# Kernel optimization log

Hardware: AMD Instinct MI355X
Metric: run time of the kernel (lower is better)

Reference implementation:

```python
import math
import jax, jax.numpy as jnp
import numpy as np

B, T, DM, H = 2, 2048, 512, 8
D = DM // H
PROB_SPARSE_FACTOR = 0.4


def setup_inputs() -> dict:
    key = jax.random.key(0)
    ks = jax.random.split(key, 11)
    s = DM ** -0.5
    return {
        "query": jax.random.normal(ks[0], (B, T, DM), jnp.float32),
        "key": jax.random.normal(ks[1], (B, T, DM), jnp.float32),
        "value": jax.random.normal(ks[2], (B, T, DM), jnp.float32),
        "Wq": jax.random.normal(ks[3], (DM, DM), jnp.float32) * s,
        "bq": jnp.zeros((DM,), jnp.float32),
        "Wk": jax.random.normal(ks[4], (DM, DM), jnp.float32) * s,
        "bk": jnp.zeros((DM,), jnp.float32),
        "Wv": jax.random.normal(ks[5], (DM, DM), jnp.float32) * s,
        "bv": jnp.zeros((DM,), jnp.float32),
        "Wo": jax.random.normal(ks[6], (DM, DM), jnp.float32) * s,
        "bo": jnp.zeros((DM,), jnp.float32),
    }


def reference(query, key, value, Wq, bq, Wk, bk, Wv, bv, Wo, bo):
    Bq, Tq, dm = query.shape
    Tk = key.shape[1]
    # projections (torch Linear: x @ W.T + b), split heads -> [B,H,T,D]
    q = (query @ Wq.T + bq).reshape(Bq, Tq, H, D).transpose(0, 2, 1, 3)
    k = (key @ Wk.T + bk).reshape(Bq, Tk, H, D).transpose(0, 2, 1, 3)
    v = (value @ Wv.T + bv).reshape(Bq, Tk, H, D).transpose(0, 2, 1, 3)
    scale = math.sqrt(D)

    # full scores for KL-based query selection
    scores_all = jnp.einsum("bhqd,bhkd->bhqk", q, k) / scale  # [B,H,Tq,Tk]
    probs = jax.nn.softmax(scores_all, axis=-1)
    log_uniform = math.log(1.0 / Tk + 1e-10)
    kl = jnp.sum(probs * (jnp.log(probs + 1e-10) - log_uniform), axis=-1)  # [B,H,Tq]

    u = int(min(PROB_SPARSE_FACTOR * math.log(Tk), Tq))  # static
    _, topk = jax.lax.top_k(kl, u)  # [B,H,u]

    # gather selected queries, reduced attention
    q_red = jnp.take_along_axis(q, topk[..., None], axis=2)  # [B,H,u,D]
    s = jnp.einsum("bhud,bhkd->bhuk", q_red, k) / scale
    s = jnp.clip(jnp.nan_to_num(s, nan=-10000.0), -10000.0, 10000.0)
    w = jax.nn.softmax(s, axis=-1)
    out_red = jnp.einsum("bhuk,bhkd->bhud", w, v)  # [B,H,u,D]

    # scatter back into zeros at selected query positions
    b_idx = jnp.arange(Bq)[:, None, None]
    h_idx = jnp.arange(H)[None, :, None]
    out = jnp.zeros((Bq, H, Tq, D), q.dtype).at[b_idx, h_idx, topk].set(out_red)

    out = out.transpose(0, 2, 1, 3).reshape(Bq, Tq, dm)
    return out @ Wo.T + bo
```

## Files before the change

kernel.cpp:

```cpp
#include <hip/hip_runtime.h>
#include <hip/hip_bf16.h>

#define TT 2048
#define DMM 512
#define HH 8
#define DH 64
#define NBH 16
#define UU 3

typedef unsigned short u16;
typedef short bf16x8 __attribute__((ext_vector_type(8)));
typedef float f32x4 __attribute__((ext_vector_type(4)));

#define W_ZS     0
#define W_SS     131072
#define W_OUTRED 262144
#define W_TOPK   265216
#define W_U16    265280
#define NPROJ 2097152
#define NW    786432
#define W_NEED_BYTES (265280*4 + 5*NPROJ*2 + 2*NW*2)

__global__ void canary_kernel(float* __restrict__ out, float code, int n)
{
    int i = blockIdx.x * 256 + threadIdx.x;
    if (i < n) out[i] = (i == 0) ? code : 0.f;
}

__device__ __forceinline__ float rc_bf(u16 hi, u16 lo)
{
    return __uint_as_float(((unsigned)hi) << 16) + __uint_as_float(((unsigned)lo) << 16);
}

__global__ __launch_bounds__(256) void wsplit_kernel(
    const float* __restrict__ Wq, const float* __restrict__ Wk,
    const float* __restrict__ Wv,
    u16* __restrict__ whi, u16* __restrict__ wlo)
{
    const int n1 = DMM * DMM;
    for (int i = blockIdx.x * 256 + threadIdx.x; i < 3 * n1; i += gridDim.x * 256) {
        const int z = i / n1, rem = i - z * n1;
        const float w = (z == 0 ? Wq : (z == 1 ? Wk : Wv))[rem];
        const unsigned u = __float_as_uint(w);
        const u16 hi = (u16)(u >> 16);
        const float hf = __uint_as_float(u & 0xFFFF0000u);
        whi[i] = hi;
        wlo[i] = (u16)(__float_as_uint(w - hf) >> 16);
    }
}

__global__ __launch_bounds__(256) void projM_kernel(
    const float* __restrict__ q, const float* __restrict__ k, const float* __restrict__ v,
    const u16* __restrict__ whi, const u16* __restrict__ wlo,
    const float* __restrict__ bq, const float* __restrict__ bk, const float* __restrict__ bv,
    u16* __restrict__ qhi, u16* __restrict__ qlo,
    u16* __restrict__ khi, u16* __restrict__ klo,
    u16* __restrict__ Vh)
{
    __shared__ u16 Ah[128][40], Al[128][40], Bh[64][40], Bl[64][40];

    const int z = blockIdx.z;
    const float *X, *Bi;
    if (z == 0)      { X = q; Bi = bq; }
    else if (z == 1) { X = k; Bi = bk; }
    else             { X = v; Bi = bv; }

    const int tid = threadIdx.x;
    const int m0 = blockIdx.x * 128;
    const int h  = blockIdx.y;
    const int n0 = h * 64;
    const int w  = tid >> 6;
    const int lane = tid & 63;
    const int fr = lane & 15;
    const int kg = lane >> 4;
    const int kb = kg * 8;

    const int sr = tid >> 1;
    const int sk = (tid & 1) * 16;
    const int wr = tid >> 2;
    const int wk = (tid & 3) * 8;

    f32x4 acc[2][4];
#pragma unroll
    for (int t = 0; t < 2; ++t)
#pragma unroll
        for (int j = 0; j < 4; ++j) acc[t][j] = (f32x4){0.f, 0.f, 0.f, 0.f};

    for (int k0 = 0; k0 < DMM; k0 += 32) {
        __syncthreads();
        {
            const float* p = X + (size_t)(m0 + sr) * DMM + k0 + sk;
            float xv[16];
#pragma unroll
            for (int i4 = 0; i4 < 4; ++i4) {
                float4 a = *(const float4*)(p + i4 * 4);
                xv[i4*4+0]=a.x; xv[i4*4+1]=a.y; xv[i4*4+2]=a.z; xv[i4*4+3]=a.w;
            }
            unsigned hb[16], lb[16];
#pragma unroll
            for (int i = 0; i < 16; ++i) {
                unsigned u = __float_as_uint(xv[i]);
                hb[i] = u >> 16;
                float hf = __uint_as_float(u & 0xFFFF0000u);
                lb[i] = __float_as_uint(xv[i] - hf) >> 16;
            }
#pragma unroll
            for (int half = 0; half < 2; ++half) {
                uint4 H, L;
                H.x = hb[half*8+0]|(hb[half*8+1]<<16); H.y = hb[half*8+2]|(hb[half*8+3]<<16);
                H.z = hb[half*8+4]|(hb[half*8+5]<<16); H.w = hb[half*8+6]|(hb[half*8+7]<<16);
                L.x = lb[half*8+0]|(lb[half*8+1]<<16); L.y = lb[half*8+2]|(lb[half*8+3]<<16);
                L.z = lb[half*8+4]|(lb[half*8+5]<<16); L.w = lb[half*8+6]|(lb[half*8+7]<<16);
                *(uint4*)&Ah[sr][sk + half*8] = H;
                *(uint4*)&Al[sr][sk + half*8] = L;
            }

            const size_t wi = ((size_t)z * DMM + n0 + wr) * DMM + k0 + wk;
            *(uint4*)&Bh[wr][wk] = *(const uint4*)(whi + wi);
            *(uint4*)&Bl[wr][wk] = *(const uint4*)(wlo + wi);
        }
        __syncthreads();

        bf16x8 ah[2], al[2];
#pragma unroll
        for (int t = 0; t < 2; ++t) {
            ah[t] = *(const bf16x8*)&Ah[w*32 + t*16 + fr][kb];
            al[t] = *(const bf16x8*)&Al[w*32 + t*16 + fr][kb];
        }
#pragma unroll
        for (int j = 0; j < 4; ++j) {
            bf16x8 bhf = *(const bf16x8*)&Bh[j*16 + fr][kb];
            bf16x8 blf = *(const bf16x8*)&Bl[j*16 + fr][kb];
#pragma unroll
            for (int t = 0; t < 2; ++t) {
                acc[t][j] = __builtin_amdgcn_mfma_f32_16x16x32_bf16(ah[t], bhf, acc[t][j], 0, 0, 0);
                acc[t][j] = __builtin_amdgcn_mfma_f32_16x16x32_bf16(ah[t], blf, acc[t][j], 0, 0, 0);
                acc[t][j] = __builtin_amdgcn_mfma_f32_16x16x32_bf16(al[t], bhf, acc[t][j], 0, 0, 0);
            }
        }
    }

#pragma unroll
    for (int t = 0; t < 2; ++t) {
#pragma unroll
        for (int j = 0; j < 4; ++j) {
            const int d = j*16 + fr;
            const float bias = Bi[n0 + d];
#pragma unroll
            for (int r = 0; r < 4; ++r) {
                const int row = m0 + w*32 + t*16 + kg*4 + r;
                const int bb  = row >> 11;
                const int tt  = row & 2047;
                const float val = acc[t][j][r] + bias;
                const size_t idx = ((size_t)(bb*HH + h) * TT + tt) * DH + d;
                const unsigned u = __float_as_uint(val);
                if (z == 2) {
                    Vh[idx] = (u16)((u + 0x7FFFu + ((u >> 16) & 1u)) >> 16);
                } else {
                    const u16 hi = (u16)(u >> 16);
                    const float hf = __uint_as_float(u & 0xFFFF0000u);
                    const u16 lo = (u16)(__float_as_uint(val - hf) >> 16);
                    if (z == 0) { qhi[idx] = hi; qlo[idx] = lo; }
                    else        { khi[idx] = hi; klo[idx] = lo; }
                }
            }
        }
    }
}

__global__ __launch_bounds__(256) void scoreM_kernel(
    const u16* __restrict__ qhi, const u16* __restrict__ qlo,
    const u16* __restrict__ khi, const u16* __restrict__ klo,
    float* __restrict__ zs, float* __restrict__ ss)
{
    __shared__ u16 Kh[64][76], Kl[64][76];

    const int qt = blockIdx.x, bh = blockIdx.y, zh = blockIdx.z;
    const int qr0 = qt * 128;
    const int tid = threadIdx.x;
    const int w  = tid >> 6;
    const int lane = tid & 63;
    const int fr = lane & 15;
    const int kg = lane >> 4;
    const int kb = kg * 8;

    bf16x8 qh0[2], qh1[2], ql0[2], ql1[2];
#pragma unroll
    for (int t = 0; t < 2; ++t) {
        const size_t qbase = ((size_t)bh*TT + qr0 + w*32 + t*16 + fr) * DH;
        qh0[t] = *(const bf16x8*)(qhi + qbase + kb);
        qh1[t] = *(const bf16x8*)(qhi + qbase + 32 + kb);
        ql0[t] = *(const bf16x8*)(qlo + qbase + kb);
        ql1[t] = *(const bf16x8*)(qlo + qbase + 32 + kb);
    }

    float zl[2][4], s1l[2][4];
#pragma unroll
    for (int t = 0; t < 2; ++t)
#pragma unroll
        for (int r = 0; r < 4; ++r) { zl[t][r] = 0.f; s1l[t][r] = 0.f; }

    const int c  = tid >> 2;
    const int dq = (tid & 3) * 16;

    for (int ct = zh * 8; ct < zh * 8 + 8; ++ct) {
        __syncthreads();
        {
            const u16* sh = khi + ((size_t)bh*TT + ct*64 + c) * DH + dq;
            const u16* sl = klo + ((size_t)bh*TT + ct*64 + c) * DH + dq;
            *(uint4*)&Kh[c][dq]     = *(const uint4*)sh;
            *(uint4*)&Kh[c][dq + 8] = *(const uint4*)(sh + 8);
            *(uint4*)&Kl[c][dq]     = *(const uint4*)sl;
            *(uint4*)&Kl[c][dq + 8] = *(const uint4*)(sl + 8);
        }
        __syncthreads();

        f32x4 acc[2][4];
#pragma unroll
        for (int t = 0; t < 2; ++t)
#pragma unroll
            for (int j = 0; j < 4; ++j) acc[t][j] = (f32x4){0.f, 0.f, 0.f, 0.f};

#pragma unroll
        for (int j = 0; j < 4; ++j) {
            const bf16x8 b0h = *(const bf16x8*)&Kh[j*16 + fr][kb];
            const bf16x8 b0l = *(const bf16x8*)&Kl[j*16 + fr][kb];
            const bf16x8 b1h = *(const bf16x8*)&Kh[j*16 + fr][32 + kb];
            const bf16x8 b1l = *(const bf16x8*)&Kl[j*16 + fr][32 + kb];
#pragma unroll
            for (int t = 0; t < 2; ++t) {
                acc[t][j] = __builtin_amdgcn_mfma_f32_16x16x32_bf16(qh0[t], b0h, acc[t][j], 0, 0, 0);
                acc[t][j] = __builtin_amdgcn_mfma_f32_16x16x32_bf16(qh0[t], b0l, acc[t][j], 0, 0, 0);
                acc[t][j] = __builtin_amdgcn_mfma_f32_16x16x32_bf16(ql0[t], b0h, acc[t][j], 0, 0, 0);
                acc[t][j] = __builtin_amdgcn_mfma_f32_16x16x32_bf16(qh1[t], b1h, acc[t][j], 0, 0, 0);
                acc[t][j] = __builtin_amdgcn_mfma_f32_16x16x32_bf16(qh1[t], b1l, acc[t][j], 0, 0, 0);
                acc[t][j] = __builtin_amdgcn_mfma_f32_16x16x32_bf16(ql1[t], b1h, acc[t][j], 0, 0, 0);
            }
        }

#pragma unroll
        for (int t = 0; t < 2; ++t) {
#pragma unroll
            for (int j = 0; j < 4; ++j) {
#pragma unroll
                for (int r = 0; r < 4; ++r) {
                    float s = acc[t][j][r] * 0.125f;
                    float e = __expf(s);
                    zl[t][r]  += e;
                    s1l[t][r] += e * s;
                }
            }
        }
    }

#pragma unroll
    for (int off = 1; off < 16; off <<= 1) {
#pragma unroll
        for (int t = 0; t < 2; ++t)
#pragma unroll
            for (int r = 0; r < 4; ++r) {
                zl[t][r]  += __shfl_xor(zl[t][r],  off, 64);
                s1l[t][r] += __shfl_xor(s1l[t][r], off, 64);
            }
    }

    if (fr == 0) {
#pragma unroll
        for (int t = 0; t < 2; ++t)
#pragma unroll
            for (int r = 0; r < 4; ++r) {
                const int row = qr0 + w*32 + t*16 + kg*4 + r;
                const size_t o = ((size_t)zh * NBH + bh) * TT + row;
                zs[o] = zl[t][r];
                ss[o] = s1l[t][r];
            }
    }
}

__global__ __launch_bounds__(256) void top3redM_kernel(
    const float* __restrict__ zs, const float* __restrict__ ss,
    const u16* __restrict__ qhi, const u16* __restrict__ qlo,
    const u16* __restrict__ khi, const u16* __restrict__ klo,
    const u16* __restrict__ Vh,
    int* __restrict__ topk, float* __restrict__ outred)
{
    __shared__ float kv[TT];
    __shared__ float pv[4];
    __shared__ int   pi[4];
    __shared__ int   tsel_sh;
    __shared__ float qs[DH];
    __shared__ float wbuf[TT];
    __shared__ float red4[4][DH];
    __shared__ float wz[4];

    const int bu = blockIdx.x;
    const int bh = bu / UU;
    const int uu = bu - bh * UU;
    const int tid = threadIdx.x;
    const int wv = tid >> 6;

    for (int i = tid; i < TT; i += 256) {
        float Z = 0.f, S = 0.f;
#pragma unroll
        for (int p = 0; p < 4; ++p) {
            const size_t o = ((size_t)p * NBH + bh) * TT + i;
            Z += zs[o];
            S += ss[o];
        }
        kv[i] = S / Z - logf(Z);
    }
    __syncthreads();
    for (int it = 0; it <= uu; ++it) {
        float bvv = -3e38f; int bi = TT;
        for (int i = tid; i < TT; i += 256) {
            float vv = kv[i];
            if (vv > bvv) { bvv = vv; bi = i; }
        }
#pragma unroll
        for (int off = 1; off < 64; off <<= 1) {
            float ov = __shfl_xor(bvv, off, 64);
            int   oi = __shfl_xor(bi, off, 64);
            if (ov > bvv || (ov == bvv && oi < bi)) { bvv = ov; bi = oi; }
        }
        if ((tid & 63) == 0) { pv[wv] = bvv; pi[wv] = bi; }
        __syncthreads();
        if (tid == 0) {
            float Bv = pv[0]; int Bi2 = pi[0];
#pragma unroll
            for (int w2 = 1; w2 < 4; ++w2) {
                if (pv[w2] > Bv || (pv[w2] == Bv && pi[w2] < Bi2)) { Bv = pv[w2]; Bi2 = pi[w2]; }
            }
            tsel_sh = Bi2;
            kv[Bi2] = -3e38f;
        }
        __syncthreads();
    }
    const int tsel = tsel_sh;
    if (tid == 0) topk[bu] = tsel;

    if (tid < DH) {
        const size_t qi = ((size_t)bh*TT + tsel) * DH + tid;
        qs[tid] = rc_bf(qhi[qi], qlo[qi]);
    }
    __syncthreads();

    float zp = 0.f;
    for (int cc = tid; cc < TT; cc += 256) {
        const u16* kh  = khi + ((size_t)bh*TT + cc) * DH;
        const u16* kl_ = klo + ((size_t)bh*TT + cc) * DH;
        float s = 0.f;
#pragma unroll
        for (int d8 = 0; d8 < DH; d8 += 8) {
            uint4 H = *(const uint4*)(kh + d8);
            uint4 L = *(const uint4*)(kl_ + d8);
            const unsigned hw[4] = {H.x, H.y, H.z, H.w};
            const unsigned lw[4] = {L.x, L.y, L.z, L.w};
#pragma unroll
            for (int i = 0; i < 4; ++i) {
                float k0 = __uint_as_float(hw[i] << 16) + __uint_as_float(lw[i] << 16);
                float k1 = __uint_as_float(hw[i] & 0xFFFF0000u) + __uint_as_float(lw[i] & 0xFFFF0000u);
                s += qs[d8 + i*2]     * k0;
                s += qs[d8 + i*2 + 1] * k1;
            }
        }
        s *= 0.125f;
        s = fminf(fmaxf(s, -10000.f), 10000.f);
        float e = __expf(s);
        wbuf[cc] = e;
        zp += e;
    }
#pragma unroll
    for (int off = 1; off < 64; off <<= 1) zp += __shfl_xor(zp, off, 64);
    if ((tid & 63) == 0) wz[wv] = zp;
    __syncthreads();
    const float Z = wz[0] + wz[1] + wz[2] + wz[3];

    const int d = tid & 63, cq = tid >> 6;
    float o = 0.f;
    for (int cc = cq * 512; cc < cq * 512 + 512; ++cc) {
        const u16 vb = Vh[((size_t)bh*TT + cc) * DH + d];
        o += wbuf[cc] * __uint_as_float(((unsigned)vb) << 16);
    }
    red4[cq][d] = o;
    __syncthreads();
    if (tid < DH)
        outred[bu*DH + tid] =
            (red4[0][tid] + red4[1][tid] + red4[2][tid] + red4[3][tid]) / Z;
}

__global__ __launch_bounds__(256) void outU_kernel(
    const float* __restrict__ outred, const int* __restrict__ topk,
    const float* __restrict__ Wo, const float* __restrict__ bo,
    float* __restrict__ out)
{
    const int blk = blockIdx.x;
    const int b   = blk >> 11;
    const int t   = blk & 2047;
    const int tid = threadIdx.x;
    float acc0 = bo[tid];
    float acc1 = bo[tid + 256];
    for (int h = 0; h < HH; ++h) {
#pragma unroll
        for (int u = 0; u < UU; ++u) {
            const int idx = (b*HH + h)*UU + u;
            if (topk[idx] == t) {
                const float* r  = outred + (size_t)idx * DH;
                const float* w0 = Wo + (size_t)tid * DMM + h*DH;
                const float* w1 = Wo + (size_t)(tid + 256) * DMM + h*DH;
#pragma unroll
                for (int dd = 0; dd < DH; ++dd) {
                    const float rv = r[dd];
                    acc0 += rv * w0[dd];
                    acc1 += rv * w1[dd];
                }
            }
        }
    }
    out[(size_t)blk * DMM + tid]       = acc0;
    out[(size_t)blk * DMM + tid + 256] = acc1;
}

extern "C" void kernel_launch(void* const* d_in, const int* in_sizes, int n_in,
                              void* d_out, int out_size, void* d_ws, size_t ws_size,
                              hipStream_t stream)
{
    float* out = (float*)d_out;
    const int nblk = (out_size + 255) / 256;

    if (n_in != 11) {
        canary_kernel<<<nblk, 256, 0, stream>>>(out, 9216.f + 8.f * (float)n_in, out_size);
        return;
    }
    const int s0 = in_sizes[0];
    int mode = -1;
    if ((s0 == 2097152 || s0 == 8388608) &&
        (in_sizes[4] == 512 || in_sizes[4] == 2048)) mode = 0;
    else if ((s0 == 262144 || s0 == 1048576) &&
             (in_sizes[8] == 2097152 || in_sizes[8] == 8388608)) mode = 1;
    if (mode < 0) {
        canary_kernel<<<nblk, 256, 0, stream>>>(out, 8192.f, out_size);
        return;
    }
    if (ws_size < (size_t)W_NEED_BYTES) {
        canary_kernel<<<nblk, 256, 0, stream>>>(out, 5120.f, out_size);
        return;
    }

    const float *q, *k, *v, *Wq, *bq, *Wk, *bk, *Wv, *bv, *Wo, *bo;
    if (mode == 0) {
        q  = (const float*)d_in[0];  k  = (const float*)d_in[1];
        v  = (const float*)d_in[2];  Wq = (const float*)d_in[3];
        bq = (const float*)d_in[4];  Wk = (const float*)d_in[5];
        bk = (const float*)d_in[6];  Wv = (const float*)d_in[7];
        bv = (const float*)d_in[8];  Wo = (const float*)d_in[9];
        bo = (const float*)d_in[10];
    } else {
        Wk = (const float*)d_in[0];  Wo = (const float*)d_in[1];
        Wq = (const float*)d_in[2];  Wv = (const float*)d_in[3];
        bk = (const float*)d_in[4];  bo = (const float*)d_in[5];
        bq = (const float*)d_in[6];  bv = (const float*)d_in[7];
        k  = (const float*)d_in[8];  q  = (const float*)d_in[9];
        v  = (const float*)d_in[10];
    }

    float* ws     = (float*)d_ws;
    float* zs     = ws + W_ZS;
    float* ss     = ws + W_SS;
    float* outred = ws + W_OUTRED;
    int*   topk   = (int*)(ws + W_TOPK);
    u16*   qhi    = (u16*)(ws + W_U16);
    u16*   qlo    = qhi + (size_t)NPROJ;
    u16*   khi    = qlo + (size_t)NPROJ;
    u16*   klo    = khi + (size_t)NPROJ;
    u16*   Vh     = klo + (size_t)NPROJ;
    u16*   whi    = Vh  + (size_t)NPROJ;
    u16*   wlo    = whi + (size_t)NW;

    wsplit_kernel<<<1024, 256, 0, stream>>>(Wq, Wk, Wv, whi, wlo);
    projM_kernel<<<dim3(32, 8, 3), 256, 0, stream>>>(q, k, v, whi, wlo, bq, bk, bv,
                                                     qhi, qlo, khi, klo, Vh);
    scoreM_kernel<<<dim3(16, 16, 4), 256, 0, stream>>>(qhi, qlo, khi, klo, zs, ss);
    top3redM_kernel<<<48, 256, 0, stream>>>(zs, ss, qhi, qlo, khi, klo, Vh, topk, outred);
    outU_kernel<<<4096, 256, 0, stream>>>(outred, topk, Wo, bo, out);
}
```

Measured before the change: 133.4 us.

## Split reduced attention over key chunks across blocks, combine partials in output kernel

```diff
diff --git a/kernel.cpp b/kernel.cpp
--- a/kernel.cpp
+++ b/kernel.cpp
@@ -7,6 +7,7 @@
 #define DH 64
 #define NBH 16
 #define UU 3
+#define NPARTS 8
 
 typedef unsigned short u16;
 typedef short bf16x8 __attribute__((ext_vector_type(8)));
@@ -14,12 +15,13 @@
 
 #define W_ZS     0
 #define W_SS     131072
-#define W_OUTRED 262144
-#define W_TOPK   265216
-#define W_U16    265280
+#define W_ZP     262144
+#define W_OP     262528
+#define W_TOPK   287104
+#define W_U16    287168
 #define NPROJ 2097152
 #define NW    786432
-#define W_NEED_BYTES (265280*4 + 5*NPROJ*2 + 2*NW*2)
+#define W_NEED_BYTES (287168*4 + 5*NPROJ*2 + 2*NW*2)
 
 __global__ void canary_kernel(float* __restrict__ out, float code, int n)
 {
@@ -282,18 +284,19 @@
     const u16* __restrict__ qhi, const u16* __restrict__ qlo,
     const u16* __restrict__ khi, const u16* __restrict__ klo,
     const u16* __restrict__ Vh,
-    int* __restrict__ topk, float* __restrict__ outred)
+    int* __restrict__ topk, float* __restrict__ zp_out, float* __restrict__ op_out)
 {
     __shared__ float kv[TT];
     __shared__ float pv[4];
     __shared__ int   pi[4];
     __shared__ int   tsel_sh;
     __shared__ float qs[DH];
-    __shared__ float wbuf[TT];
+    __shared__ float wbuf[256];
     __shared__ float red4[4][DH];
     __shared__ float wz[4];
 
     const int bu = blockIdx.x;
+    const int part = blockIdx.y;
     const int bh = bu / UU;
     const int uu = bu - bh * UU;
     const int tid = threadIdx.x;
@@ -336,7 +339,7 @@
         __syncthreads();
     }
     const int tsel = tsel_sh;
-    if (tid == 0) topk[bu] = tsel;
+    if (tid == 0 && part == 0) topk[bu] = tsel;
 
     if (tid < DH) {
         const size_t qi = ((size_t)bh*TT + tsel) * DH + tid;
@@ -344,8 +347,9 @@
     }
     __syncthreads();
 
-    float zp = 0.f;
-    for (int cc = tid; cc < TT; cc += 256) {
+    const int c0 = part * 256;
+    const int cc = c0 + tid;
+    {
         const u16* kh  = khi + ((size_t)bh*TT + cc) * DH;
         const u16* kl_ = klo + ((size_t)bh*TT + cc) * DH;
         float s = 0.f;
@@ -366,30 +370,33 @@
         s *= 0.125f;
         s = fminf(fmaxf(s, -10000.f), 10000.f);
         float e = __expf(s);
-        wbuf[cc] = e;
-        zp += e;
-    }
-#pragma unroll
-    for (int off = 1; off < 64; off <<= 1) zp += __shfl_xor(zp, off, 64);
-    if ((tid & 63) == 0) wz[wv] = zp;
+        wbuf[tid] = e;
+        float zp = e;
+#pragma unroll
+        for (int off = 1; off < 64; off <<= 1) zp += __shfl_xor(zp, off, 64);
+        if ((tid & 63) == 0) wz[wv] = zp;
+    }
     __syncthreads();
-    const float Z = wz[0] + wz[1] + wz[2] + wz[3];
+    if (tid == 0) zp_out[bu*NPARTS + part] = wz[0] + wz[1] + wz[2] + wz[3];
 
     const int d = tid & 63, cq = tid >> 6;
     float o = 0.f;
-    for (int cc = cq * 512; cc < cq * 512 + 512; ++cc) {
-        const u16 vb = Vh[((size_t)bh*TT + cc) * DH + d];
-        o += wbuf[cc] * __uint_as_float(((unsigned)vb) << 16);
+#pragma unroll
+    for (int i = 0; i < 64; ++i) {
+        const int ii = cq * 64 + i;
+        const u16 vb = Vh[((size_t)bh*TT + c0 + ii) * DH + d];
+        o += wbuf[ii] * __uint_as_float(((unsigned)vb) << 16);
     }
     red4[cq][d] = o;
     __syncthreads();
     if (tid < DH)
-        outred[bu*DH + tid] =
-            (red4[0][tid] + red4[1][tid] + red4[2][tid] + red4[3][tid]) / Z;
+        op_out[(size_t)(bu*NPARTS + part) * DH + tid] =
+            red4[0][tid] + red4[1][tid] + red4[2][tid] + red4[3][tid];
 }
 
 __global__ __launch_bounds__(256) void outU_kernel(
-    const float* __restrict__ outred, const int* __restrict__ topk,
+    const float* __restrict__ zp, const float* __restrict__ op,
+    const int* __restrict__ topk,
     const float* __restrict__ Wo, const float* __restrict__ bo,
     float* __restrict__ out)
 {
@@ -404,12 +411,19 @@
         for (int u = 0; u < UU; ++u) {
             const int idx = (b*HH + h)*UU + u;
             if (topk[idx] == t) {
-                const float* r  = outred + (size_t)idx * DH;
+                float Z = 0.f;
+#pragma unroll
+                for (int p = 0; p < NPARTS; ++p) Z += zp[idx*NPARTS + p];
+                const float invz = 1.0f / Z;
+                const float* ob = op + (size_t)idx * NPARTS * DH;
                 const float* w0 = Wo + (size_t)tid * DMM + h*DH;
                 const float* w1 = Wo + (size_t)(tid + 256) * DMM + h*DH;
 #pragma unroll
                 for (int dd = 0; dd < DH; ++dd) {
-                    const float rv = r[dd];
+                    float rv = 0.f;
+#pragma unroll
+                    for (int p = 0; p < NPARTS; ++p) rv += ob[p*DH + dd];
+                    rv *= invz;
                     acc0 += rv * w0[dd];
                     acc1 += rv * w1[dd];
                 }
@@ -466,7 +480,8 @@
     float* ws     = (float*)d_ws;
     float* zs     = ws + W_ZS;
     float* ss     = ws + W_SS;
-    float* outred = ws + W_OUTRED;
+    float* zp     = ws + W_ZP;
+    float* op     = ws + W_OP;
     int*   topk   = (int*)(ws + W_TOPK);
     u16*   qhi    = (u16*)(ws + W_U16);
     u16*   qlo    = qhi + (size_t)NPROJ;
@@ -480,6 +495,7 @@
     projM_kernel<<<dim3(32, 8, 3), 256, 0, stream>>>(q, k, v, whi, wlo, bq, bk, bv,
                                                      qhi, qlo, khi, klo, Vh);
     scoreM_kernel<<<dim3(16, 16, 4), 256, 0, stream>>>(qhi, qlo, khi, klo, zs, ss);
-    top3redM_kernel<<<48, 256, 0, stream>>>(zs, ss, qhi, qlo, khi, klo, Vh, topk, outred);
-    outU_kernel<<<4096, 256, 0, stream>>>(outred, topk, Wo, bo, out);
-}
+    top3redM_kernel<<<dim3(48, NPARTS), 256, 0, stream>>>(zs, ss, qhi, qlo, khi, klo, Vh,
+                                                          topk, zp, op);
+    outU_kernel<<<4096, 256, 0, stream>>>(zp, op, topk, Wo, bo, out);
+}
```

Result: faster. 110.3 us (median of 2 runs) (-17.3%).
